# Performance work log

Hardware: AMD Instinct MI355X
Metric: run time of the kernel (lower is better)

The kernel has to match this reference:

```python
import jax, jax.numpy as jnp
import numpy as np

FEATURE_DIM = 128  # user_aae.feature_dim == item_aae.feature_dim


def _encode(row, W1, b1, W2, b2):
    # row = [feature | x_rest]; original concatenates x and feature before the encoder MLP
    feat = row[:, :FEATURE_DIM]
    xr = row[:, FEATURE_DIM:]
    h = jax.nn.relu(jnp.concatenate([xr, feat], axis=-1) @ W1 + b1)
    return h @ W2 + b2  # [B, latent]


def setup_inputs() -> dict:
    key = jax.random.key(0)
    ks = jax.random.split(key, 12)
    B, NU, NI = 8192, 50000, 50000
    ROW, H, L = 2128, 512, 256  # feature_dim(128) + x_dim(2000)
    x = jnp.stack([
        jax.random.randint(ks[0], (B,), 0, NU),
        jax.random.randint(ks[1], (B,), 0, NI),
    ], axis=1).astype(jnp.int64)
    s1 = 1.0 / np.sqrt(ROW)
    s2 = 1.0 / np.sqrt(H)
    return {
        "x": x,
        "user_lookup": jax.random.normal(ks[2], (NU, ROW), jnp.float32),
        "item_lookup": jax.random.normal(ks[3], (NI, ROW), jnp.float32),
        "uW1": jax.random.normal(ks[4], (ROW, H), jnp.float32) * s1,
        "ub1": jnp.zeros((H,), jnp.float32),
        "uW2": jax.random.normal(ks[5], (H, L), jnp.float32) * s2,
        "ub2": jnp.zeros((L,), jnp.float32),
        "iW1": jax.random.normal(ks[6], (ROW, H), jnp.float32) * s1,
        "ib1": jnp.zeros((H,), jnp.float32),
        "iW2": jax.random.normal(ks[7], (H, L), jnp.float32) * s2,
        "ib2": jnp.zeros((L,), jnp.float32),
    }


def reference(x, user_lookup, item_lookup, uW1, ub1, uW2, ub2, iW1, ib1, iW2, ib2):
    user_row = user_lookup[x[:, 0]]  # [B, ROW]
    item_row = item_lookup[x[:, 1]]  # [B, ROW]
    u = _encode(user_row, uW1, ub1, uW2, ub2)  # [B, L]
    v = _encode(item_row, iW1, ib1, iW2, ib2)  # [B, L]
    # diag(u @ v.T) == rowwise dot product (identical math, no B x B matrix)
    diag = jnp.sum(u * v, axis=-1)
    return diag[:, None]  # [B, 1]
```

## Files before the change

### kernel.cpp

```cpp
#include <hip/hip_runtime.h>
#include <stdint.h>

typedef __attribute__((ext_vector_type(8))) short bf16x8;
typedef __attribute__((ext_vector_type(4))) float f32x4;

#define MFMA16(a, b, c) __builtin_amdgcn_mfma_f32_16x16x32_bf16((a), (b), (c), 0, 0, 0)

static __device__ __forceinline__ unsigned short f2bf(float f) {
  union { float f; unsigned int u; } cv;
  cv.f = f;
  return (unsigned short)((cv.u + 0x7fffu + ((cv.u >> 16) & 1u)) >> 16);
}

#define BATCH 8192
#define ROWD  2128
#define HID   512
#define LATD  256
#define KC1   272
#define NT1   68
#define HSL_TW (BATCH * HID)

__global__ __launch_bounds__(256) void ASAECF_tcast(
    const float* __restrict__ in0, const float* __restrict__ in1,
    unsigned short* __restrict__ out, int N, int lgN, int Kin, int KC, int perm)
{
  const float* __restrict__ in = blockIdx.z ? in1 : in0;
  unsigned short* __restrict__ o = out + (size_t)blockIdx.z * KC * N * 8;
  const int s = blockIdx.x * 256 + threadIdx.x;
  const int kc = s >> lgN, n = s & (N - 1);
  unsigned short v[8];
#pragma unroll
  for (int e = 0; e < 8; ++e) {
    const int k = kc * 8 + e;
    float f = 0.0f;
    if (k < Kin) {
      const int src = perm ? (k < 128 ? k + 2000 : k - 128) : k;
      f = in[(size_t)src * N + n];
    }
    v[e] = f2bf(f);
  }
  *(uint4*)(o + (size_t)s * 8) = *(const uint4*)v;
}

__global__ __launch_bounds__(512) void ASAECF_gemm1(
    const int* __restrict__ x,
    const float* __restrict__ ulook, const float* __restrict__ ilook,
    const unsigned short* __restrict__ w1s,
    const float* __restrict__ ub1, const float* __restrict__ ib1,
    unsigned short* __restrict__ hsl)
{
  const int bid   = blockIdx.x;
  const int xcd   = bid & 7;
  const int tower = xcd >> 2;
  const int rb    = (bid >> 3) * 4 + (xcd & 3);

  const float* __restrict__ look = tower ? ilook : ulook;
  const unsigned short* __restrict__ w1 = w1s + (size_t)tower * KC1 * HID * 8;
  const float* __restrict__ b1 = tower ? ib1 : ub1;
  unsigned short* __restrict__ hout = hsl + (size_t)tower * HSL_TW;

  __shared__ unsigned short Ab[2][64 * 40];

  const int tid  = threadIdx.x;
  const int lane = tid & 63, wid = tid >> 6;
  const int fr   = lane & 15, fq = lane >> 4;
  const int row0 = rb * 64;

  const int ar = tid >> 3, ak = (tid & 7) * 4;
  const long long arow = (long long)x[(row0 + ar) * 2 + tower] * ROWD + ak;

  int boff[4];
#pragma unroll
  for (int n = 0; n < 4; ++n)
    boff[n] = (fq * 512 + wid * 64 + n * 16 + fr) * 8;

  auto loadA = [&](int tt) -> f32x4 {
    f32x4 v = {0.0f, 0.0f, 0.0f, 0.0f};
    if (tt * 32 + ak <= ROWD - 4)
      v = __builtin_nontemporal_load((const f32x4*)(look + arow + tt * 32));
    return v;
  };
  auto writeA = [&](int buf, f32x4 v) {
    uint2 p;
    p.x = (unsigned)f2bf(v[0]) | ((unsigned)f2bf(v[1]) << 16);
    p.y = (unsigned)f2bf(v[2]) | ((unsigned)f2bf(v[3]) << 16);
    *(uint2*)&Ab[buf][ar * 40 + ak] = p;
  };

  f32x4 acc[4][4] = {};
  bf16x8 bgc[4], bgn[4];
  f32x4 rA0, rA1;

  writeA(0, loadA(0));
  rA0 = loadA(1);
  rA1 = loadA(2);
#pragma unroll
  for (int n = 0; n < 4; ++n) bgc[n] = *(const bf16x8*)(w1 + boff[n]);

#pragma unroll 2
  for (int t = 0; t < NT1; ++t) {
    __syncthreads();
    const int cu = t & 1;

    const unsigned short* bpn = w1 + (size_t)(t + 1) * (4 * 512 * 8);
#pragma unroll
    for (int n = 0; n < 4; ++n) bgn[n] = *(const bf16x8*)(bpn + boff[n]);

    bf16x8 af[4];
#pragma unroll
    for (int m = 0; m < 4; ++m)
      af[m] = *(const bf16x8*)&Ab[cu][(m * 16 + fr) * 40 + fq * 8];
#pragma unroll
    for (int n = 0; n < 4; ++n)
#pragma unroll
      for (int m = 0; m < 4; ++m)
        acc[m][n] = MFMA16(af[m], bgc[n], acc[m][n]);

    if (cu == 0) { writeA(1, rA0); rA0 = loadA(t + 3); }
    else         { writeA(0, rA1); rA1 = loadA(t + 3); }

#pragma unroll
    for (int n = 0; n < 4; ++n) bgc[n] = bgn[n];
  }

#pragma unroll
  for (int n = 0; n < 4; ++n) {
    const int col = wid * 64 + n * 16 + fr;
    const int kc = col >> 3, e = col & 7;
    const float bb = b1[col];
    unsigned short* hb = hout + (((size_t)rb * 64 + kc) * 64) * 8 + e;
#pragma unroll
    for (int m = 0; m < 4; ++m)
#pragma unroll
      for (int i = 0; i < 4; ++i) {
        const int row = m * 16 + fq * 4 + i;
        const float v = fmaxf(acc[m][n][i] + bb, 0.0f);
        hb[row * 8] = f2bf(v);
      }
  }
}

__global__ __launch_bounds__(512, 2) void ASAECF_gemm2dot(
    const unsigned short* __restrict__ hsl,
    const unsigned short* __restrict__ w2s,
    const float* __restrict__ ub2, const float* __restrict__ ib2,
    float* __restrict__ out)
{
  const int tid  = threadIdx.x;
  const int lane = tid & 63, wid = tid >> 6;
  const int fr   = lane & 15, fq = lane >> 4;
  const int rb   = blockIdx.x;
  const int row0 = rb * 32;

  const unsigned short* __restrict__ hu = hsl;
  const unsigned short* __restrict__ hv = hsl + (size_t)HSL_TW;
  const size_t abase = ((size_t)(rb >> 1) * 64) * 64 * 8;
  const int lrow0 = (rb & 1) * 32;

  f32x4 au[2][2] = {}, av[2][2] = {};

#pragma unroll
  for (int t = 0; t < 8; ++t) {
#pragma unroll
    for (int s = 0; s < 2; ++s) {
      const int kc = t * 8 + s * 4 + fq;
      bf16x8 a_u[2], a_v[2], b_u[2], b_v[2];
#pragma unroll
      for (int m = 0; m < 2; ++m) {
        const size_t off = abase + ((size_t)kc * 64 + lrow0 + m * 16 + fr) * 8;
        a_u[m] = *(const bf16x8*)(hu + off);
        a_v[m] = *(const bf16x8*)(hv + off);
      }
#pragma unroll
      for (int n = 0; n < 2; ++n) {
        const int col = wid * 32 + n * 16 + fr;
        const size_t offb = ((size_t)kc * 256 + col) * 8;
        b_u[n] = *(const bf16x8*)(w2s + offb);
        b_v[n] = *(const bf16x8*)(w2s + (size_t)64 * 256 * 8 + offb);
      }
#pragma unroll
      for (int m = 0; m < 2; ++m)
#pragma unroll
        for (int n = 0; n < 2; ++n) {
          au[m][n] = MFMA16(a_u[m], b_u[n], au[m][n]);
          av[m][n] = MFMA16(a_v[m], b_v[n], av[m][n]);
        }
    }
  }

  __shared__ float red[8][32];
  float bu[2], bv[2];
#pragma unroll
  for (int n = 0; n < 2; ++n) {
    const int col = wid * 32 + n * 16 + fr;
    bu[n] = ub2[col];
    bv[n] = ib2[col];
  }
#pragma unroll
  for (int m = 0; m < 2; ++m)
#pragma unroll
    for (int i = 0; i < 4; ++i) {
      float p = 0.0f;
#pragma unroll
      for (int n = 0; n < 2; ++n)
        p += (au[m][n][i] + bu[n]) * (av[m][n][i] + bv[n]);
      p += __shfl_xor(p, 1, 64);
      p += __shfl_xor(p, 2, 64);
      p += __shfl_xor(p, 4, 64);
      p += __shfl_xor(p, 8, 64);
      if (fr == 0) red[wid][m * 16 + fq * 4 + i] = p;
    }
  __syncthreads();
  if (tid < 32) {
    float s = 0.0f;
#pragma unroll
    for (int w = 0; w < 8; ++w) s += red[w][tid];
    out[row0 + tid] = s;
  }
}

extern "C" void kernel_launch(void* const* d_in, const int* in_sizes, int n_in,
                              void* d_out, int out_size, void* d_ws, size_t ws_size,
                              hipStream_t stream) {
  (void)in_sizes; (void)n_in; (void)out_size; (void)ws_size;
  const int*   x     = (const int*)d_in[0];
  const float* ulook = (const float*)d_in[1];
  const float* ilook = (const float*)d_in[2];
  const float* uW1   = (const float*)d_in[3];
  const float* ub1   = (const float*)d_in[4];
  const float* uW2   = (const float*)d_in[5];
  const float* ub2   = (const float*)d_in[6];
  const float* iW1   = (const float*)d_in[7];
  const float* ib1   = (const float*)d_in[8];
  const float* iW2   = (const float*)d_in[9];
  const float* ib2   = (const float*)d_in[10];
  float* out = (float*)d_out;

  char* ws = (char*)d_ws;
  unsigned short* w1s = (unsigned short*)(ws);
  unsigned short* w2s = (unsigned short*)(ws + 4456448);
  unsigned short* hsl = (unsigned short*)(ws + 4980736);

  ASAECF_tcast<<<dim3(544, 1, 2), 256, 0, stream>>>(uW1, iW1, w1s, 512, 9, ROWD, KC1, 1);
  ASAECF_tcast<<<dim3(64, 1, 2),  256, 0, stream>>>(uW2, iW2, w2s, 256, 8, HID, 64, 0);
  ASAECF_gemm1<<<dim3(256), 512, 0, stream>>>(x, ulook, ilook, w1s, ub1, ib1, hsl);
  ASAECF_gemm2dot<<<dim3(256), 512, 0, stream>>>(hsl, w2s, ub2, ib2, out);
}
```

Measured before the change: 89.37 us.

## Split gemm1 output columns across two blocks to double grid size

```diff
diff --git a/kernel.cpp b/kernel.cpp
--- a/kernel.cpp
+++ b/kernel.cpp
@@ -6,10 +6,10 @@
 
 #define MFMA16(a, b, c) __builtin_amdgcn_mfma_f32_16x16x32_bf16((a), (b), (c), 0, 0, 0)
 
-static __device__ __forceinline__ unsigned short f2bf(float f) {
-  union { float f; unsigned int u; } cv;
+static __device__ __forceinline__ unsigned f2bf(float f) {
+  union { float f; unsigned u; } cv;
   cv.f = f;
-  return (unsigned short)((cv.u + 0x7fffu + ((cv.u >> 16) & 1u)) >> 16);
+  return (cv.u + 0x7fffu + ((cv.u >> 16) & 1u)) >> 16;
 }
 
 #define BATCH 8192
@@ -37,12 +37,12 @@
       const int src = perm ? (k < 128 ? k + 2000 : k - 128) : k;
       f = in[(size_t)src * N + n];
     }
-    v[e] = f2bf(f);
+    v[e] = (unsigned short)f2bf(f);
   }
   *(uint4*)(o + (size_t)s * 8) = *(const uint4*)v;
 }
 
-__global__ __launch_bounds__(512) void ASAECF_gemm1(
+__global__ __launch_bounds__(512, 4) void ASAECF_gemm1(
     const int* __restrict__ x,
     const float* __restrict__ ulook, const float* __restrict__ ilook,
     const unsigned short* __restrict__ w1s,
@@ -51,8 +51,10 @@
 {
   const int bid   = blockIdx.x;
   const int xcd   = bid & 7;
+  const int idx   = bid >> 3;
   const int tower = xcd >> 2;
-  const int rb    = (bid >> 3) * 4 + (xcd & 3);
+  const int nh    = idx & 1;
+  const int mb    = (xcd & 3) * 32 + (idx >> 1);
 
   const float* __restrict__ look = tower ? ilook : ulook;
   const unsigned short* __restrict__ w1 = w1s + (size_t)tower * KC1 * HID * 8;
@@ -63,8 +65,9 @@
 
   const int tid  = threadIdx.x;
   const int lane = tid & 63, wid = tid >> 6;
+  const int wm   = wid >> 2, wn = wid & 3;
   const int fr   = lane & 15, fq = lane >> 4;
-  const int row0 = rb * 64;
+  const int row0 = mb * 64;
 
   const int ar = tid >> 3, ak = (tid & 7) * 4;
   const long long arow = (long long)x[(row0 + ar) * 2 + tower] * ROWD + ak;
@@ -72,22 +75,22 @@
   int boff[4];
 #pragma unroll
   for (int n = 0; n < 4; ++n)
-    boff[n] = (fq * 512 + wid * 64 + n * 16 + fr) * 8;
+    boff[n] = (fq * 512 + nh * 256 + wn * 64 + n * 16 + fr) * 8;
 
   auto loadA = [&](int tt) -> f32x4 {
     f32x4 v = {0.0f, 0.0f, 0.0f, 0.0f};
     if (tt * 32 + ak <= ROWD - 4)
-      v = __builtin_nontemporal_load((const f32x4*)(look + arow + tt * 32));
+      v = *(const f32x4*)(look + arow + tt * 32);
     return v;
   };
   auto writeA = [&](int buf, f32x4 v) {
     uint2 p;
-    p.x = (unsigned)f2bf(v[0]) | ((unsigned)f2bf(v[1]) << 16);
-    p.y = (unsigned)f2bf(v[2]) | ((unsigned)f2bf(v[3]) << 16);
+    p.x = f2bf(v[0]) | (f2bf(v[1]) << 16);
+    p.y = f2bf(v[2]) | (f2bf(v[3]) << 16);
     *(uint2*)&Ab[buf][ar * 40 + ak] = p;
   };
 
-  f32x4 acc[4][4] = {};
+  f32x4 acc[2][4] = {};
   bf16x8 bgc[4], bgn[4];
   f32x4 rA0, rA1;
 
@@ -106,14 +109,14 @@
 #pragma unroll
     for (int n = 0; n < 4; ++n) bgn[n] = *(const bf16x8*)(bpn + boff[n]);
 
-    bf16x8 af[4];
-#pragma unroll
-    for (int m = 0; m < 4; ++m)
-      af[m] = *(const bf16x8*)&Ab[cu][(m * 16 + fr) * 40 + fq * 8];
+    bf16x8 af[2];
+#pragma unroll
+    for (int m = 0; m < 2; ++m)
+      af[m] = *(const bf16x8*)&Ab[cu][(wm * 32 + m * 16 + fr) * 40 + fq * 8];
 #pragma unroll
     for (int n = 0; n < 4; ++n)
 #pragma unroll
-      for (int m = 0; m < 4; ++m)
+      for (int m = 0; m < 2; ++m)
         acc[m][n] = MFMA16(af[m], bgc[n], acc[m][n]);
 
     if (cu == 0) { writeA(1, rA0); rA0 = loadA(t + 3); }
@@ -125,17 +128,17 @@
 
 #pragma unroll
   for (int n = 0; n < 4; ++n) {
-    const int col = wid * 64 + n * 16 + fr;
+    const int col = nh * 256 + wn * 64 + n * 16 + fr;
     const int kc = col >> 3, e = col & 7;
     const float bb = b1[col];
-    unsigned short* hb = hout + (((size_t)rb * 64 + kc) * 64) * 8 + e;
-#pragma unroll
-    for (int m = 0; m < 4; ++m)
+    unsigned short* hb = hout + (((size_t)mb * 64 + kc) * 64) * 8 + e;
+#pragma unroll
+    for (int m = 0; m < 2; ++m)
 #pragma unroll
       for (int i = 0; i < 4; ++i) {
-        const int row = m * 16 + fq * 4 + i;
+        const int row = wm * 32 + m * 16 + fq * 4 + i;
         const float v = fmaxf(acc[m][n][i] + bb, 0.0f);
-        hb[row * 8] = f2bf(v);
+        hb[row * 8] = (unsigned short)f2bf(v);
       }
   }
 }
@@ -243,6 +246,6 @@
 
   ASAECF_tcast<<<dim3(544, 1, 2), 256, 0, stream>>>(uW1, iW1, w1s, 512, 9, ROWD, KC1, 1);
   ASAECF_tcast<<<dim3(64, 1, 2),  256, 0, stream>>>(uW2, iW2, w2s, 256, 8, HID, 64, 0);
-  ASAECF_gemm1<<<dim3(256), 512, 0, stream>>>(x, ulook, ilook, w1s, ub1, ib1, hsl);
+  ASAECF_gemm1<<<dim3(512), 512, 0, stream>>>(x, ulook, ilook, w1s, ub1, ib1, hsl);
   ASAECF_gemm2dot<<<dim3(256), 512, 0, stream>>>(hsl, w2s, ub2, ib2, out);
 }
```

Result: slower. 95.17 us (+6.5%).
